# Optimization experiments

Hardware: AMD Instinct MI355X
Metric: run time of the kernel (lower is better)

## Reference

```python
import jax, jax.numpy as jnp
import numpy as np

N_NODES = 50000
N_EDGES = 800000
N_GRAPHS = 64


def _gatv2_conv(x, src, dst, edge_attr, Wl, bl, Wr, br, We, att, bias):
    """PyG GATv2Conv (concat=True, negative_slope=0.2, share_weights=False)."""
    N = x.shape[0]
    H, C = att.shape
    x_l = (x @ Wl + bl).reshape(N, H, C)   # source transform (messages)
    x_r = (x @ Wr + br).reshape(N, H, C)   # target transform
    e = (edge_attr @ We).reshape(-1, H, C)  # [E,H,C] edge embedding
    m = jax.nn.leaky_relu(x_l[src] + x_r[dst] + e, 0.2)   # [E,H,C]
    score = jnp.einsum('ehc,hc->eh', m, att)               # [E,H]
    # segment softmax over incoming edges of each target node
    smax = jax.ops.segment_max(score, dst, num_segments=N)
    ex = jnp.exp(score - smax[dst])
    den = jax.ops.segment_sum(ex, dst, num_segments=N)
    alpha = ex / (den[dst] + 1e-16)                        # [E,H]
    out = jax.ops.segment_sum(alpha[..., None] * x_l[src], dst, num_segments=N)
    return out.reshape(N, H * C) + bias


def setup_inputs() -> dict:
    key = jax.random.key(0)
    ks = jax.random.split(key, 20)
    s = lambda k, shape, fan: jax.random.normal(k, shape, jnp.float32) * (1.0 / np.sqrt(fan))
    inp = {
        'x': jax.random.normal(ks[0], (N_NODES, 128), jnp.float32),
        'edge_attr': jax.random.normal(ks[1], (N_EDGES, 16), jnp.float32),
        'edge_index': jax.random.randint(ks[2], (2, N_EDGES), 0, N_NODES),
        'batch': jnp.sort(jax.random.randint(ks[3], (N_NODES,), 0, N_GRAPHS)),
        # layer 0: in=128 -> heads=4, C=64 (out 256)
        'Wl0': s(ks[4], (128, 256), 128), 'bl0': jnp.zeros((256,), jnp.float32),
        'Wr0': s(ks[5], (128, 256), 128), 'br0': jnp.zeros((256,), jnp.float32),
        'We0': s(ks[6], (16, 256), 16),
        'att0': s(ks[7], (4, 64), 64),
        'bias0': jnp.zeros((256,), jnp.float32),
        # layer 1: in=256 -> heads=4, C=32 (out 128)
        'Wl1': s(ks[8], (256, 128), 256), 'bl1': jnp.zeros((128,), jnp.float32),
        'Wr1': s(ks[9], (256, 128), 256), 'br1': jnp.zeros((128,), jnp.float32),
        'We1': s(ks[10], (16, 128), 16),
        'att1': s(ks[11], (4, 32), 32),
        'bias1': jnp.zeros((128,), jnp.float32),
        'fc1W': s(ks[12], (128, 128), 128), 'fc1b': jnp.zeros((128,), jnp.float32),
        'fc2W': s(ks[13], (128, 1), 128), 'fc2b': jnp.zeros((1,), jnp.float32),
    }
    return inp


def reference(x, edge_attr, edge_index, batch,
              Wl0, bl0, Wr0, br0, We0, att0, bias0,
              Wl1, bl1, Wr1, br1, We1, att1, bias1,
              fc1W, fc1b, fc2W, fc2b):
    src, dst = edge_index[0], edge_index[1]
    h = _gatv2_conv(x, src, dst, edge_attr, Wl0, bl0, Wr0, br0, We0, att0, bias0)
    h = jax.nn.relu(h)  # dropout is identity (training=False)
    h = _gatv2_conv(h, src, dst, edge_attr, Wl1, bl1, Wr1, br1, We1, att1, bias1)
    h = jax.nn.relu(h)
    # global mean pool over graphs
    pooled = jax.ops.segment_sum(h, batch, num_segments=N_GRAPHS)
    cnt = jax.ops.segment_sum(jnp.ones((h.shape[0],), h.dtype), batch, num_segments=N_GRAPHS)
    pooled = pooled / jnp.maximum(cnt, 1.0)[:, None]
    z = jax.nn.relu(pooled @ fc1W + fc1b)
    z = z @ fc2W + fc2b
    return jax.nn.sigmoid(z)
```

## Files before the change

### kernel.cpp

```cpp
#include <hip/hip_runtime.h>
#include <hip/hip_bf16.h>

typedef unsigned int  u32;
typedef unsigned short u16;
typedef __attribute__((ext_vector_type(8))) short bf16x8;
typedef __attribute__((ext_vector_type(4))) float f32x4;
typedef __attribute__((ext_vector_type(2))) float f32x2;
typedef _Float16 f16;
typedef __attribute__((ext_vector_type(2))) _Float16 f16x2;

__device__ __forceinline__ float bfbits(u32 u){ union{u32 i; float f;} v; v.i=u; return v.f; }
__device__ __forceinline__ float bf2f(u16 u){ return bfbits(((u32)u)<<16); }
__device__ __forceinline__ u16 f2bf(float f){
  union{float f; u32 i;} v; v.f=f;
  u32 r = v.i + 0x7FFFu + ((v.i>>16)&1u);
  return (u16)(r>>16);
}
__device__ __forceinline__ u16 f2h_bits(float f){
  union{ f16 h; u16 u; } v; v.h=(f16)f; return v.u;
}
__device__ __forceinline__ f16x2 as_h2(u32 u){ union{u32 u; f16x2 h;} v; v.u=u; return v.h; }
__device__ __forceinline__ int clampi(int v, int lo, int hi){ return v<lo?lo:(v>hi?hi:v); }
__device__ __forceinline__ f32x2 unpack2(u32 q){
  f32x2 r; r.x = bfbits(q<<16); r.y = bfbits(q&0xFFFF0000u); return r;
}

#if defined(__has_builtin)
#if __has_builtin(__builtin_amdgcn_fdot2)
#define USE_FDOT2 1
#endif
#if __has_builtin(__builtin_amdgcn_update_dpp)
#define USE_DPP 1
#endif
#endif

__device__ __forceinline__ float dot2acc(u32 a, u32 b, float c){
#ifdef USE_FDOT2
  return __builtin_amdgcn_fdot2(as_h2(a), as_h2(b), c, false);
#else
  f16x2 ha = as_h2(a), hb = as_h2(b);
  return c + (float)ha.x*(float)hb.x + (float)ha.y*(float)hb.y;
#endif
}

__device__ __forceinline__ float row_reduce16(float x){
#ifdef USE_DPP
  union{float f; int i;} u, t;
  u.f = x; t.i = __builtin_amdgcn_update_dpp(0, u.i, 0x121, 0xF, 0xF, true); x += t.f;
  u.f = x; t.i = __builtin_amdgcn_update_dpp(0, u.i, 0x122, 0xF, 0xF, true); x += t.f;
  u.f = x; t.i = __builtin_amdgcn_update_dpp(0, u.i, 0x124, 0xF, 0xF, true); x += t.f;
  u.f = x; t.i = __builtin_amdgcn_update_dpp(0, u.i, 0x128, 0xF, 0xF, true); x += t.f;
  return x;
#else
  x += __shfl_xor(x,1); x += __shfl_xor(x,2);
  x += __shfl_xor(x,4); x += __shfl_xor(x,8);
  return x;
#endif
}

__global__ void detect_kernel(const u16* __restrict__ xr, int* __restrict__ flag){
  __shared__ int cnt;
  if (threadIdx.x==0) cnt=0;
  __syncthreads();
  int c=0;
  for (int i=threadIdx.x; i<8192; i+=256){
    u16 u = xr[i];
    int e = (u>>7)&0xFF;
    if (e>=0x90 || u==0) c++;
  }
  atomicAdd(&cnt, c);
  __syncthreads();
  if (threadIdx.x==0) *flag = (cnt>16) ? 1 : 0;
}

__device__ __forceinline__ float rdin(const void* p, int idx, int f){
  return f ? ((const float*)p)[idx] : bf2f(((const u16*)p)[idx]);
}

__global__ void canon_big(const void* __restrict__ xr, const void* __restrict__ ear,
                          const int* __restrict__ flag,
                          ushort4* __restrict__ xbf, ushort4* __restrict__ eabf,
                          int NX4, int NE4){
  int f = *flag;
  if (!f) return;
  int i = blockIdx.x*blockDim.x + threadIdx.x;
  if (i < NX4){
    const float4 v = ((const float4*)xr)[i];
    ushort4 o; o.x=f2bf(v.x); o.y=f2bf(v.y); o.z=f2bf(v.z); o.w=f2bf(v.w);
    xbf[i]=o;
  } else if (i < NX4+NE4){
    int j = i - NX4;
    const float4 v = ((const float4*)ear)[j];
    ushort4 o; o.x=f2bf(v.x); o.y=f2bf(v.y); o.z=f2bf(v.z); o.w=f2bf(v.w);
    eabf[j]=o;
  }
}

__global__ void canon_small(const int* __restrict__ flag,
   const void* Wl0, const void* Wr0, const void* Wl1, const void* Wr1,
   const void* We0, const void* We1,
   const void* bl0, const void* br0, const void* bias0, const void* att0,
   const void* bl1, const void* br1, const void* bias1, const void* att1,
   const void* fc1b, const void* fc2W, const void* fc2b, const void* fc1W,
   u16* __restrict__ wbf, u32* __restrict__ we0p, u32* __restrict__ we1p,
   float* __restrict__ params, int* __restrict__ deg, int N)
{
  int f = *flag;
  int i = blockIdx.x*blockDim.x + threadIdx.x;
  if (i < N) deg[i] = 0;
  if (i < 32768){
    { int c=i>>7, k=i&127;
      wbf[i]        = f2bf(rdin(Wl0, k*256+c, f));
      wbf[32768+i]  = f2bf(rdin(Wr0, k*256+c, f)); }
    { int c=i>>8, k=i&255;
      wbf[65536+i]  = f2bf(rdin(Wl1, k*128+c, f));
      wbf[98304+i]  = f2bf(rdin(Wr1, k*128+c, f)); }
  }
  if (i < 2048){ int c=i&255, p=i>>8;
    float lo = rdin(We0, (2*p)*256 + c, f);
    float hi = rdin(We0, (2*p+1)*256 + c, f);
    we0p[c*8+p] = (u32)f2h_bits(lo) | ((u32)f2h_bits(hi)<<16);
  }
  if (i < 1024){ int c=i&127, p=i>>7;
    float lo = rdin(We1, (2*p)*128 + c, f);
    float hi = rdin(We1, (2*p+1)*128 + c, f);
    we1p[c*8+p] = (u32)f2h_bits(lo) | ((u32)f2h_bits(hi)<<16);
  }
  if (i < 256){ params[i]=rdin(bl0,i,f); params[256+i]=rdin(br0,i,f);
                params[512+i]=rdin(bias0,i,f); params[768+i]=rdin(att0,i,f); }
  if (i < 128){ params[1024+i]=rdin(bl1,i,f); params[1152+i]=rdin(br1,i,f);
                params[1280+i]=rdin(bias1,i,f); params[1408+i]=rdin(att1,i,f);
                params[1536+i]=rdin(fc1b,i,f); params[1664+i]=rdin(fc2W,i,f); }
  if (i == 0) params[1792] = rdin(fc2b,0,f);
  if (i < 16384) params[1800+i] = rdin(fc1W,i,f);
}

__global__ void hist_kernel(const int* __restrict__ ei, int* __restrict__ deg, int E, int N){
  int e = blockIdx.x*blockDim.x + threadIdx.x;
  if (e < E) atomicAdd(&deg[clampi(ei[E+e],0,N-1)], 1);
}

__global__ __launch_bounds__(1024) void scan1_kernel(const int* __restrict__ deg,
    int* __restrict__ incl, int* __restrict__ bsum, int n){
  __shared__ int lds[1024];
  int t = threadIdx.x;
  int i = blockIdx.x*1024 + t;
  int v = (i<n)? deg[i] : 0;
  lds[t]=v;
  __syncthreads();
  for (int off=1; off<1024; off<<=1){
    int add = (t>=off)? lds[t-off] : 0;
    __syncthreads();
    lds[t] += add;
    __syncthreads();
  }
  if (i<n) incl[i]=lds[t];
  if (t==1023) bsum[blockIdx.x]=lds[1023];
}
__global__ __launch_bounds__(1024) void scan2_kernel(int* __restrict__ bsum, int NB){
  __shared__ int lds[1024];
  int t = threadIdx.x;
  int v = (t<NB)? bsum[t] : 0;
  lds[t]=v;
  __syncthreads();
  for (int off=1; off<1024; off<<=1){
    int add = (t>=off)? lds[t-off] : 0;
    __syncthreads();
    lds[t] += add;
    __syncthreads();
  }
  if (t<NB) bsum[t] = lds[t]-v;
}
__global__ __launch_bounds__(1024) void scan3_kernel(const int* __restrict__ incl,
    const int* __restrict__ bsum, int* __restrict__ indptr, int* __restrict__ deg, int n){
  int i = blockIdx.x*1024 + threadIdx.x;
  if (i<n){
    int inc = incl[i], d = deg[i];
    int ex = bsum[blockIdx.x] + inc - d;
    indptr[i] = ex;
    deg[i] = 0;
    if (i==n-1) indptr[n] = ex + d;
  }
}

__global__ void scatter_kernel(const int* __restrict__ ei, const int* __restrict__ indptr,
                               int* __restrict__ fill, int* __restrict__ eid, int E, int N){
  int e = blockIdx.x*blockDim.x + threadIdx.x;
  if (e < E){
    int d = clampi(ei[E+e], 0, N-1);
    int pos = clampi(indptr[d] + atomicAdd(&fill[d], 1), 0, E-1);
    eid[pos] = e;
  }
}

__global__ void csr_payload(const int* __restrict__ eid, const int* __restrict__ ei,
                            const u16* __restrict__ eabf, const void* __restrict__ ea_orig,
                            const int* __restrict__ flag,
                            int* __restrict__ csr_src, u32* __restrict__ ea_csr, int E, int N){
  const u16* src = (*flag) ? eabf : (const u16*)ea_orig;
  int pos = blockIdx.x*blockDim.x + threadIdx.x;
  if (pos < E){
    int e = clampi(eid[pos], 0, E-1);
    csr_src[pos] = clampi(ei[e], 0, N-1);
    const uint4* q = (const uint4*)(src + (size_t)e*16);
    uint4 a = q[0], b = q[1];
    u32 in[8] = {a.x,a.y,a.z,a.w,b.x,b.y,b.z,b.w};
    u32 o[8];
    #pragma unroll
    for (int k=0;k<8;k++){
      f32x2 p = unpack2(in[k]);
      o[k] = (u32)f2h_bits(p.x) | ((u32)f2h_bits(p.y)<<16);
    }
    uint4* op = (uint4*)(ea_csr + (size_t)pos*8);
    op[0] = make_uint4(o[0],o[1],o[2],o[3]);
    op[1] = make_uint4(o[4],o[5],o[6],o[7]);
  } else if (pos < E+64){
    csr_src[pos] = 0;
    uint4* op = (uint4*)(ea_csr + (size_t)pos*8);
    op[0] = make_uint4(0,0,0,0);
    op[1] = make_uint4(0,0,0,0);
  }
}

template<int K, int M, int MT>
__global__ __launch_bounds__(256) void node_gemm(
    const u16* __restrict__ Xc, const void* __restrict__ xorig, const int* __restrict__ flag,
    const u16* __restrict__ WlT, const float* __restrict__ blf,
    const u16* __restrict__ WrT, const float* __restrict__ brf,
    u16* __restrict__ XL, u16* __restrict__ XR, int N)
{
  constexpr int KS = K/32;
  constexpr int NCT = 2*M/16;
  const u16* X = (flag && !*flag) ? (const u16*)xorig : Xc;
  int wave = threadIdx.x >> 6, lane = threadIdx.x & 63;
  int kq = (lane >> 4) * 8;
  int mbase = blockIdx.x*MT*16;

  bf16x8 af[MT][KS];
  #pragma unroll
  for (int r=0; r<MT; r++){
    int m = mbase + r*16 + (lane & 15);
    if (m >= N) m = N-1;
    const u16* xrow = X + (size_t)m*K;
    #pragma unroll
    for (int s=0; s<KS; s++) af[r][s] = *(const bf16x8*)(xrow + s*32 + kq);
  }

  for (int ct = wave; ct < NCT; ct += 4){
    int col = ct*16 + (lane & 15);
    bool isR = (col >= M);
    int c = isR ? col - M : col;
    const u16* WT = isR ? WrT : WlT;
    float bv = isR ? brf[c] : blf[c];
    u16* OUT = isR ? XR : XL;
    bf16x8 bfr[KS];
    const u16* wrow = WT + (size_t)c*K;
    #pragma unroll
    for (int s=0; s<KS; s++) bfr[s] = *(const bf16x8*)(wrow + s*32 + kq);
    #pragma unroll
    for (int r=0; r<MT; r++){
      f32x4 acc = {0.f,0.f,0.f,0.f};
      #pragma unroll
      for (int s=0; s<KS; s++)
        acc = __builtin_amdgcn_mfma_f32_16x16x32_bf16(af[r][s], bfr[s], acc, 0,0,0);
      #pragma unroll
      for (int q=0; q<4; q++){
        int node = mbase + r*16 + (lane>>4)*4 + q;
        if (node < N) OUT[(size_t)node*M + c] = f2bf(acc[q] + bv);
      }
    }
  }
}

template<int M, int CH>
__global__ __launch_bounds__(256) void fused_score_agg(
    const int* __restrict__ indptr, const int* __restrict__ csr_src,
    const u32* __restrict__ eaP,
    const u32* __restrict__ weP, const u16* __restrict__ xl,
    const u16* __restrict__ xr, const float* __restrict__ attf,
    const float* __restrict__ biasf, u16* __restrict__ outp, int N, int E)
{
  constexpr int VPT = M/64;
  constexpr int VP2 = VPT/2;
  constexpr int C = M/4;
  int wvi = threadIdx.x>>6;
  int lane = threadIdx.x & 63;
  int c0 = lane*VPT;
  int h = lane>>4;

  u32 wp[8][VPT];
  #pragma unroll
  for (int c=0;c<VPT;c++){
    uint4 q0 = *(const uint4*)(weP + (u32)(c0+c)*8);
    uint4 q1 = *(const uint4*)(weP + (u32)(c0+c)*8 + 4);
    wp[0][c]=q0.x; wp[1][c]=q0.y; wp[2][c]=q0.z; wp[3][c]=q0.w;
    wp[4][c]=q1.x; wp[5][c]=q1.y; wp[6][c]=q1.z; wp[7][c]=q1.w;
  }
  float atv[VPT], bvv[VPT];
  #pragma unroll
  for (int c=0;c<VPT;c++){ atv[c] = attf[h*C + ((c0&(C-1)) + c)]; bvv[c] = biasf[c0+c]; }

  int nquads = (N+3)>>2;
  for (int nb = blockIdx.x; nb < nquads; nb += gridDim.x){
  int n = nb*4 + wvi;
  if (n < N){

  float xrv[VPT];
  if constexpr (VPT==4){
    uint2 q = *(const uint2*)(xr + (u32)n*M + c0);
    f32x2 a = unpack2(q.x), b = unpack2(q.y);
    xrv[0]=a.x; xrv[1]=a.y; xrv[2]=b.x; xrv[3]=b.y;
  } else {
    u32 q = *(const u32*)(xr + (u32)n*M + c0);
    f32x2 a = unpack2(q);
    xrv[0]=a.x; xrv[1]=a.y;
  }

  int s0 = clampi(indptr[n],0,E), s1 = clampi(indptr[n+1],s0,E);

  float m = -1e30f, d = 0.f;
  f32x2 acc2[VP2];
  #pragma unroll
  for (int q=0;q<VP2;q++) acc2[q] = (f32x2){0.f,0.f};

  struct Buf {
    int   src[CH];
    uint4 ea0[CH], ea1[CH];
    uint2 x4[CH];
    u32   x2[CH];
  };
  Buf A, B;

  auto loadSrc = [&](Buf& Bf, int base){
    #pragma unroll
    for (int j=0;j<CH;j++) Bf.src[j] = csr_src[base+j];
  };
  auto loadEA = [&](Buf& Bf, int base){
    #pragma unroll
    for (int j=0;j<CH;j++){
      const uint4* qp = (const uint4*)(eaP + (u32)(base+j)*8);
      Bf.ea0[j]=qp[0]; Bf.ea1[j]=qp[1];
    }
  };
  auto gath = [&](Buf& Bf){
    #pragma unroll
    for (int j=0;j<CH;j++){
      u32 off = (u32)Bf.src[j]*M + c0;
      if constexpr (VPT==4) Bf.x4[j] = *(const uint2*)(xl + off);
      else                  Bf.x2[j] = *(const u32*)(xl + off);
    }
  };
  auto computeC = [&](Buf& Bf, int base){
    int cnt = s1-base; if (cnt>CH) cnt=CH;
    f32x2 xlv2[CH][VP2];
    float pj[CH];
    #pragma unroll
    for (int j=0;j<CH;j++){
      if constexpr (VPT==4){
        xlv2[j][0] = unpack2(Bf.x4[j].x); xlv2[j][1] = unpack2(Bf.x4[j].y);
      } else {
        xlv2[j][0] = unpack2(Bf.x2[j]);
      }
      float s[VPT];
      #pragma unroll
      for (int c=0;c<VPT;c++){
        float xlc = (c&1) ? xlv2[j][c>>1].y : xlv2[j][c>>1].x;
        s[c] = xlc + xrv[c];
      }
      #pragma unroll
      for (int c=0;c<VPT;c++){
        s[c] = dot2acc(Bf.ea0[j].x, wp[0][c], s[c]);
        s[c] = dot2acc(Bf.ea0[j].y, wp[1][c], s[c]);
        s[c] = dot2acc(Bf.ea0[j].z, wp[2][c], s[c]);
        s[c] = dot2acc(Bf.ea0[j].w, wp[3][c], s[c]);
        s[c] = dot2acc(Bf.ea1[j].x, wp[4][c], s[c]);
        s[c] = dot2acc(Bf.ea1[j].y, wp[5][c], s[c]);
        s[c] = dot2acc(Bf.ea1[j].z, wp[6][c], s[c]);
        s[c] = dot2acc(Bf.ea1[j].w, wp[7][c], s[c]);
      }
      float pp = 0.f;
      #pragma unroll
      for (int c=0;c<VPT;c++){
        float v = s[c];
        float lv = fmaxf(v, 0.2f*v);
        pp = fmaf(lv, atv[c], pp);
      }
      pp = row_reduce16(pp);
      pj[j] = (j<cnt)? pp : -1e30f;
    }
    float mn = m;
    #pragma unroll
    for (int j=0;j<CH;j++) mn = fmaxf(mn, pj[j]);
    float sc = __expf(m - mn);
    float wvv[CH];
    #pragma unroll
    for (int j=0;j<CH;j++) wvv[j] = __expf(pj[j]-mn);
    float dd = d*sc;
    #pragma unroll
    for (int j=0;j<CH;j++) dd += wvv[j];
    d = dd;
    f32x2 scv = {sc,sc};
    #pragma unroll
    for (int q=0;q<VP2;q++){
      f32x2 a = acc2[q]*scv;
      #pragma unroll
      for (int j=0;j<CH;j++){
        f32x2 wj = {wvv[j], wvv[j]};
        a = __builtin_elementwise_fma(wj, xlv2[j][q], a);
      }
      acc2[q] = a;
    }
    m = mn;
  };

  int nch = (s1 - s0 + CH - 1)/CH;
  if (nch > 0){
    loadSrc(A, s0);
    gath(A);
    loadEA(A, s0);
    if (nch > 1) loadSrc(B, s0+CH);
    int ci = 0;
    while (true){
      int baseA = s0 + ci*CH;
      if (ci+1 < nch){ gath(B); loadEA(B, baseA+CH); }
      if (ci+2 < nch)  loadSrc(A, baseA+2*CH);
      computeC(A, baseA);
      ci++;
      if (ci >= nch) break;
      int baseB = s0 + ci*CH;
      if (ci+1 < nch){ gath(A); loadEA(A, baseB+CH); }
      if (ci+2 < nch)  loadSrc(B, baseB+2*CH);
      computeC(B, baseB);
      ci++;
      if (ci >= nch) break;
    }
  }
  float rd = 1.f/(d + 1e-16f);
  f32x2 rdv = {rd, rd};
  u16* op = outp + (u32)n*M + c0;
  #pragma unroll
  for (int q=0;q<VP2;q++){
    f32x2 bb; bb.x = bvv[2*q]; bb.y = bvv[2*q+1];
    f32x2 o = __builtin_elementwise_fma(acc2[q], rdv, bb);
    o = __builtin_elementwise_max(o, (f32x2){0.f,0.f});
    u32 pk = ((u32)f2bf(o.y)<<16) | (u32)f2bf(o.x);
    *(u32*)(op + 2*q) = pk;
  }
  }
  }
}

__device__ __forceinline__ int lower_bound_dev(const int* a, int n, int key){
  int lo=0, hi=n;
  while (lo<hi){ int mid=(lo+hi)>>1; if (a[mid] < key) lo=mid+1; else hi=mid; }
  return lo;
}

__global__ __launch_bounds__(128) void pool_mlp_kernel(
    const u16* __restrict__ h2, const int* __restrict__ batch,
    const float* __restrict__ params, const int* __restrict__ flag,
    void* __restrict__ out, int N)
{
  int g = blockIdx.x, t = threadIdx.x;
  __shared__ int sh_lo, sh_hi;
  if (t==0) sh_lo = lower_bound_dev(batch, N, g);
  if (t==1) sh_hi = lower_bound_dev(batch, N, g+1);
  __syncthreads();
  int lo = clampi(sh_lo, 0, N), hi = clampi(sh_hi, lo, N);
  float s0=0.f,s1=0.f,s2=0.f,s3=0.f,s4=0.f,s5=0.f,s6=0.f,s7=0.f;
  int n = lo;
  for (; n+8<=hi; n+=8){
    s0 += bf2f(h2[(size_t)(n+0)*128 + t]);
    s1 += bf2f(h2[(size_t)(n+1)*128 + t]);
    s2 += bf2f(h2[(size_t)(n+2)*128 + t]);
    s3 += bf2f(h2[(size_t)(n+3)*128 + t]);
    s4 += bf2f(h2[(size_t)(n+4)*128 + t]);
    s5 += bf2f(h2[(size_t)(n+5)*128 + t]);
    s6 += bf2f(h2[(size_t)(n+6)*128 + t]);
    s7 += bf2f(h2[(size_t)(n+7)*128 + t]);
  }
  for (; n<hi; n++) s0 += bf2f(h2[(size_t)n*128 + t]);
  float s = ((s0+s1)+(s2+s3)) + ((s4+s5)+(s6+s7));
  float cnt = (float)(hi-lo);
  float pooled = s / fmaxf(cnt, 1.f);
  __shared__ float pl[128];
  pl[t] = pooled;
  __syncthreads();
  const float* fc1W = params + 1800;
  float z = 0.f;
  for (int k=0; k<128; k++) z += pl[k]*fc1W[k*128 + t];
  z += params[1536 + t];
  z = (z>0.f)? z : 0.f;
  __shared__ float red[128];
  red[t] = z * params[1664 + t];
  __syncthreads();
  for (int st=64; st>0; st>>=1){
    if (t<st) red[t] += red[t+st];
    __syncthreads();
  }
  if (t==0){
    float zz = red[0] + params[1792];
    float r = 1.f/(1.f + __expf(-zz));
    if (*flag) ((float*)out)[g] = r;
    else       ((u16*)out)[g] = f2bf(r);
  }
}

extern "C" void kernel_launch(void* const* d_in, const int* in_sizes, int n_in,
                              void* d_out, int out_size, void* d_ws, size_t ws_size,
                              hipStream_t stream)
{
  const void* x     = d_in[0];
  const void* eattr = d_in[1];
  const int*  ei    = (const int*)d_in[2];
  const int*  batch = (const int*)d_in[3];

  int N = in_sizes[0] / 128;
  int E = in_sizes[2] / 2;
  int G = out_size;

  char* w = (char*)d_ws;
  int*   flag    = (int*)(w);
  int*   deg     = (int*)(w + 256);
  int*   indptr  = (int*)(w + 200448);
  int*   csr_src = (int*)(w + 400512);
  u32*   we0p    = (u32*)(w + 3601664);
  u32*   we1p    = (u32*)(w + 3610624);
  float* params  = (float*)(w + 3658240);
  u16*   wbf     = (u16*)(w + 3731200);
  u16*   xbf     = (u16*)(w + 3993600);
  u16*   eabf    = (u16*)(w + 16793600);
  u16*   xl0     = (u16*)(w + 42393600);
  u16*   xr0     = (u16*)(w + 67993600);
  u16*   h1      = (u16*)(w + 93593600);
  u16*   h2      = (u16*)(w + 119193600);
  u32*   ea_csr  = (u32*)(w + 131993600);
  int*   eid     = (int*)(w + 183193600);
  int*   incl    = (int*)(w + 186400000);
  int*   bsum    = (int*)(w + 186700032);

  detect_kernel<<<1, 256, 0, stream>>>((const u16*)x, flag);

  int NX4 = N*128/4, NE4 = E*16/4;
  canon_big<<<(NX4+NE4+255)/256, 256, 0, stream>>>(x, eattr, flag,
      (ushort4*)xbf, (ushort4*)eabf, NX4, NE4);
  canon_small<<<(N+255)/256, 256, 0, stream>>>(flag,
      d_in[4], d_in[6], d_in[11], d_in[13],
      d_in[8], d_in[15],
      d_in[5], d_in[7], d_in[10], d_in[9],
      d_in[12], d_in[14], d_in[17], d_in[16],
      d_in[19], d_in[20], d_in[21], d_in[18],
      wbf, we0p, we1p, params, deg, N);

  hist_kernel<<<(E+255)/256, 256, 0, stream>>>(ei, deg, E, N);
  int NB = (N + 1023)/1024;
  scan1_kernel<<<NB, 1024, 0, stream>>>(deg, incl, bsum, N);
  scan2_kernel<<<1, 1024, 0, stream>>>(bsum, NB);
  scan3_kernel<<<NB, 1024, 0, stream>>>(incl, bsum, indptr, deg, N);
  scatter_kernel<<<(E+255)/256, 256, 0, stream>>>(ei, indptr, deg, eid, E, N);
  csr_payload<<<(E+64+255)/256, 256, 0, stream>>>(eid, ei, eabf, eattr, flag,
      csr_src, ea_csr, E, N);

  int mt = (N+15)/16;
  int fgrid = 2048;
  node_gemm<128,256,4><<<(mt+3)/4, 256, 0, stream>>>(xbf, x, flag,
      wbf, params, wbf+32768, params+256, xl0, xr0, N);
  fused_score_agg<256,4><<<fgrid, 256, 0, stream>>>(indptr, csr_src, ea_csr,
      we0p, xl0, xr0, params+768, params+512, h1, N, E);

  node_gemm<256,128,2><<<(mt+1)/2, 256, 0, stream>>>(h1, nullptr, nullptr,
      wbf+65536, params+1024, wbf+98304, params+1152, xl0, xr0, N);
  fused_score_agg<128,4><<<fgrid, 256, 0, stream>>>(indptr, csr_src, ea_csr,
      we1p, xl0, xr0, params+1408, params+1280, h2, N, E);

  pool_mlp_kernel<<<G, 128, 0, stream>>>(h2, batch, params, flag, d_out, N);
}
```

Baseline: 697.4 us.

## Stage neighbor feature gathers into LDS via global_load_lds DMA

```diff
diff --git a/kernel.cpp b/kernel.cpp
--- a/kernel.cpp
+++ b/kernel.cpp
@@ -31,6 +31,9 @@
 #endif
 #if __has_builtin(__builtin_amdgcn_update_dpp)
 #define USE_DPP 1
+#endif
+#if __has_builtin(__builtin_amdgcn_global_load_lds)
+#define USE_GLL 1
 #endif
 #endif
 
@@ -288,6 +291,10 @@
   int c0 = lane*VPT;
   int h = lane>>4;
 
+#ifdef USE_GLL
+  __shared__ u16 sxl[4][2][CH*M];
+#endif
+
   u32 wp[8][VPT];
   #pragma unroll
   for (int c=0;c<VPT;c++){
@@ -326,8 +333,10 @@
   struct Buf {
     int   src[CH];
     uint4 ea0[CH], ea1[CH];
+#ifndef USE_GLL
     uint2 x4[CH];
     u32   x2[CH];
+#endif
   };
   Buf A, B;
 
@@ -342,25 +351,62 @@
       Bf.ea0[j]=qp[0]; Bf.ea1[j]=qp[1];
     }
   };
-  auto gath = [&](Buf& Bf){
+  auto stage = [&](Buf& Bf, int half){
+#ifdef USE_GLL
+    u16* lbase = &sxl[wvi][half][0];
+    if constexpr (VPT==4){
+      #pragma unroll
+      for (int e2=0; e2<CH/2; e2++){
+        int sj = (lane&32) ? Bf.src[e2*2+1] : Bf.src[e2*2];
+        u32 off = (u32)sj*M + (lane&31)*8;
+        __builtin_amdgcn_global_load_lds(
+          (const __attribute__((address_space(1))) void*)(xl + off),
+          (__attribute__((address_space(3))) void*)(lbase + e2*2*M),
+          16, 0, 0);
+      }
+    } else {
+      int lo = (lane&16) ? Bf.src[1] : Bf.src[0];
+      int hi = (lane&16) ? Bf.src[3] : Bf.src[2];
+      int sj = (lane&32) ? hi : lo;
+      u32 off = (u32)sj*M + (lane&15)*8;
+      __builtin_amdgcn_global_load_lds(
+        (const __attribute__((address_space(1))) void*)(xl + off),
+        (__attribute__((address_space(3))) void*)lbase,
+        16, 0, 0);
+    }
+#else
+    (void)half;
     #pragma unroll
     for (int j=0;j<CH;j++){
       u32 off = (u32)Bf.src[j]*M + c0;
       if constexpr (VPT==4) Bf.x4[j] = *(const uint2*)(xl + off);
       else                  Bf.x2[j] = *(const u32*)(xl + off);
     }
+#endif
   };
-  auto computeC = [&](Buf& Bf, int base){
+  auto computeC = [&](Buf& Bf, int base, int half){
+    (void)half;
     int cnt = s1-base; if (cnt>CH) cnt=CH;
     f32x2 xlv2[CH][VP2];
     float pj[CH];
     #pragma unroll
     for (int j=0;j<CH;j++){
+#ifdef USE_GLL
+      const u16* lb = &sxl[wvi][half][0];
+      if constexpr (VPT==4){
+        uint2 q = *(const uint2*)(lb + j*M + c0);
+        xlv2[j][0] = unpack2(q.x); xlv2[j][1] = unpack2(q.y);
+      } else {
+        u32 q = *(const u32*)(lb + j*M + c0);
+        xlv2[j][0] = unpack2(q);
+      }
+#else
       if constexpr (VPT==4){
         xlv2[j][0] = unpack2(Bf.x4[j].x); xlv2[j][1] = unpack2(Bf.x4[j].y);
       } else {
         xlv2[j][0] = unpack2(Bf.x2[j]);
       }
+#endif
       float s[VPT];
       #pragma unroll
       for (int c=0;c<VPT;c++){
@@ -416,21 +462,21 @@
   int nch = (s1 - s0 + CH - 1)/CH;
   if (nch > 0){
     loadSrc(A, s0);
-    gath(A);
+    stage(A, 0);
     loadEA(A, s0);
     if (nch > 1) loadSrc(B, s0+CH);
     int ci = 0;
     while (true){
       int baseA = s0 + ci*CH;
-      if (ci+1 < nch){ gath(B); loadEA(B, baseA+CH); }
+      if (ci+1 < nch){ stage(B, 1); loadEA(B, baseA+CH); }
       if (ci+2 < nch)  loadSrc(A, baseA+2*CH);
-      computeC(A, baseA);
+      computeC(A, baseA, 0);
       ci++;
       if (ci >= nch) break;
       int baseB = s0 + ci*CH;
-      if (ci+1 < nch){ gath(A); loadEA(A, baseB+CH); }
+      if (ci+1 < nch){ stage(A, 0); loadEA(A, baseB+CH); }
       if (ci+2 < nch)  loadSrc(B, baseB+2*CH);
-      computeC(B, baseB);
+      computeC(B, baseB, 1);
       ci++;
       if (ci >= nch) break;
     }
```

After: 1.172 ms. 1.68x slower.
